# Kernel optimization log

Measured on AMD Instinct MI355X. Metric: run time of the kernel, lower is better.

The kernel has to match this reference:

```python
import jax, jax.numpy as jnp
import numpy as np

TEMPERATURE = 0.5
EPS = 1e-8  # torch CosineSimilarity eps


def setup_inputs() -> dict:
    key = jax.random.key(0)
    # x holds 2*batch_size concatenated embeddings (two augmented views)
    x = jax.random.normal(key, (4096, 512), dtype=jnp.float32)
    return {"x": x}


def reference(x) -> jnp.ndarray:
    n2 = x.shape[0]          # 2N rows
    n = n2 // 2
    # cosine similarity: normalize rows (clamped norm as in torch), then GEMM
    norms = jnp.maximum(jnp.linalg.norm(x, axis=1, keepdims=True), EPS)
    xn = x / norms
    sim = jnp.einsum('id,jd->ij', xn, xn) / TEMPERATURE  # [2N, 2N]
    # positive logit for row i is sim[i, (i+N) mod 2N]
    idx = jnp.arange(n2)
    pos = sim[idx, (idx + n) % n2]
    # CE with label 0 over logits = [pos, negatives]; since the logit set for
    # row i is exactly {sim[i, j] : j != i}, CE_i = logsumexp_{j!=i} sim[i,j] - pos_i
    sim_masked = jnp.where(jnp.eye(n2, dtype=bool), -jnp.inf, sim)
    lse = jax.nn.logsumexp(sim_masked, axis=1)
    # criterion uses reduction='sum' then divides by bsz -> mean
    return jnp.mean(lse - pos)
```

## Files before the change

kernel.cpp:

```cpp
#include <hip/hip_runtime.h>
#include <hip/hip_bf16.h>
#include <math.h>

typedef __bf16 bf16_t;
typedef __bf16 bf16x8 __attribute__((ext_vector_type(8)));
typedef float f32x4 __attribute__((ext_vector_type(4)));

#define N2 4096
#define NHALF 2048
#define DIM 512
#define TEMP_INV 2.0f

__global__ __launch_bounds__(256) void k_prep(const float* __restrict__ x,
                                              bf16_t* __restrict__ xn,
                                              float* __restrict__ pos,
                                              float* __restrict__ diag,
                                              float* __restrict__ rowsum) {
    const int pair = blockIdx.x * 4 + (threadIdx.x >> 6);
    const int lane = threadIdx.x & 63;
    const int rowi = pair;
    const int rowp = pair + NHALF;

    const float4* xi = reinterpret_cast<const float4*>(x + (size_t)rowi * DIM);
    const float4* xp = reinterpret_cast<const float4*>(x + (size_t)rowp * DIM);
    float4 a0 = xi[lane * 2], a1 = xi[lane * 2 + 1];
    float4 b0 = xp[lane * 2], b1 = xp[lane * 2 + 1];

    float ssi = a0.x*a0.x + a0.y*a0.y + a0.z*a0.z + a0.w*a0.w
              + a1.x*a1.x + a1.y*a1.y + a1.z*a1.z + a1.w*a1.w;
    float ssp = b0.x*b0.x + b0.y*b0.y + b0.z*b0.z + b0.w*b0.w
              + b1.x*b1.x + b1.y*b1.y + b1.z*b1.z + b1.w*b1.w;
    float dot = a0.x*b0.x + a0.y*b0.y + a0.z*b0.z + a0.w*b0.w
              + a1.x*b1.x + a1.y*b1.y + a1.z*b1.z + a1.w*b1.w;
#pragma unroll
    for (int off = 32; off; off >>= 1) {
        ssi += __shfl_xor(ssi, off, 64);
        ssp += __shfl_xor(ssp, off, 64);
        dot += __shfl_xor(dot, off, 64);
    }
    const float ni = fmaxf(sqrtf(ssi), 1e-8f);
    const float np = fmaxf(sqrtf(ssp), 1e-8f);
    const float sci = 1.0f / ni, scp = 1.0f / np;

    float va[8] = {a0.x, a0.y, a0.z, a0.w, a1.x, a1.y, a1.z, a1.w};
    float vb[8] = {b0.x, b0.y, b0.z, b0.w, b1.x, b1.y, b1.z, b1.w};
    bf16x8 oi, op;
    float dii = 0.0f, dpp = 0.0f;
#pragma unroll
    for (int t = 0; t < 8; ++t) {
        oi[t] = (bf16_t)(va[t] * sci);
        op[t] = (bf16_t)(vb[t] * scp);
        float fi = (float)oi[t], fp_ = (float)op[t];
        dii += fi * fi;
        dpp += fp_ * fp_;
    }
    *reinterpret_cast<bf16x8*>(xn + (size_t)rowi * DIM + lane * 8) = oi;
    *reinterpret_cast<bf16x8*>(xn + (size_t)rowp * DIM + lane * 8) = op;
#pragma unroll
    for (int off = 32; off; off >>= 1) {
        dii += __shfl_xor(dii, off, 64);
        dpp += __shfl_xor(dpp, off, 64);
    }
    if (lane == 0) {
        const float pv = TEMP_INV * dot * sci * scp;
        pos[rowi] = pv;
        pos[rowp] = pv;
        diag[rowi] = TEMP_INV * dii;
        diag[rowp] = TEMP_INV * dpp;
    }
    if (threadIdx.x < 8) rowsum[blockIdx.x * 8 + threadIdx.x] = 0.0f;
}

__device__ __forceinline__ void load_lds16(const bf16_t* g, bf16_t* l) {
    __builtin_amdgcn_global_load_lds(
        (const __attribute__((address_space(1))) unsigned int*)g,
        (__attribute__((address_space(3))) unsigned int*)l,
        16, 0, 0);
}

__global__ __launch_bounds__(256) void k_simgemm(const bf16_t* __restrict__ xn,
                                                 float* __restrict__ rowsum) {
    __shared__ bf16_t As[128 * 32];
    __shared__ bf16_t Bs[128 * 32];
    __shared__ float  rpA[128];
    __shared__ float  rpB[128];

    const int t = blockIdx.x;
    int bn = (int)((sqrtf(8.0f * (float)t + 1.0f) - 1.0f) * 0.5f);
    while ((bn * (bn + 1)) / 2 > t) --bn;
    while (((bn + 1) * (bn + 2)) / 2 <= t) ++bn;
    const int bm = t - (bn * (bn + 1)) / 2;
    const bool diagb = (bm == bn);

    const int tid  = threadIdx.x;
    const int lane = tid & 63;
    const int wid  = tid >> 6;
    const int wr   = wid >> 1;
    const int wc   = wid & 1;
    const int q    = lane >> 4;
    const int l15  = lane & 15;

    if (tid < 128) { rpA[tid] = 0.0f; rpB[tid] = 0.0f; }

    const int sRow = tid >> 2;
    const int sCol = (tid & 3) * 8;
    const bf16_t* gA0 = xn + (size_t)(bm * 128 + sRow) * DIM + sCol;
    const bf16_t* gB0 = xn + (size_t)(bn * 128 + sRow) * DIM + sCol;
    bf16_t* lA0 = &As[tid * 8];
    bf16_t* lA1 = &As[2048 + tid * 8];
    bf16_t* lB0 = &Bs[tid * 8];
    bf16_t* lB1 = &Bs[2048 + tid * 8];

    f32x4 acc[4][4] = {};

    for (int k0 = 0; k0 < DIM; k0 += 32) {
        __syncthreads();
        load_lds16(gA0 + k0, lA0);
        load_lds16(gA0 + (size_t)64 * DIM + k0, lA1);
        load_lds16(gB0 + k0, lB0);
        load_lds16(gB0 + (size_t)64 * DIM + k0, lB1);
        __syncthreads();

        bf16x8 af[4], bf[4];
#pragma unroll
        for (int mt = 0; mt < 4; ++mt)
            af[mt] = *reinterpret_cast<const bf16x8*>(
                &As[(wr * 64 + mt * 16 + l15) * 32 + q * 8]);
#pragma unroll
        for (int nt = 0; nt < 4; ++nt)
            bf[nt] = *reinterpret_cast<const bf16x8*>(
                &Bs[(wc * 64 + nt * 16 + l15) * 32 + q * 8]);
#pragma unroll
        for (int mt = 0; mt < 4; ++mt)
#pragma unroll
            for (int nt = 0; nt < 4; ++nt)
                acc[mt][nt] = __builtin_amdgcn_mfma_f32_16x16x32_bf16(
                    af[mt], bf[nt], acc[mt][nt], 0, 0, 0);
    }

    float colacc[4] = {0.0f, 0.0f, 0.0f, 0.0f};
#pragma unroll
    for (int mt = 0; mt < 4; ++mt) {
        float rowp[4] = {0.0f, 0.0f, 0.0f, 0.0f};
#pragma unroll
        for (int nt = 0; nt < 4; ++nt)
#pragma unroll
            for (int r = 0; r < 4; ++r) {
                float e = __expf(TEMP_INV * acc[mt][nt][r]);
                rowp[r] += e;
                colacc[nt] += e;
            }
#pragma unroll
        for (int r = 0; r < 4; ++r) {
            float p = rowp[r];
            p += __shfl_xor(p, 1, 64);
            p += __shfl_xor(p, 2, 64);
            p += __shfl_xor(p, 4, 64);
            p += __shfl_xor(p, 8, 64);
            if (l15 == 0) atomicAdd(&rpA[wr * 64 + mt * 16 + q * 4 + r], p);
        }
    }
    if (!diagb) {
#pragma unroll
        for (int nt = 0; nt < 4; ++nt) {
            float c = colacc[nt];
            c += __shfl_xor(c, 16, 64);
            c += __shfl_xor(c, 32, 64);
            if (q == 0) atomicAdd(&rpB[wc * 64 + nt * 16 + l15], c);
        }
    }
    __syncthreads();
    if (tid < 128) {
        atomicAdd(&rowsum[bm * 128 + tid], rpA[tid]);
    } else if (!diagb) {
        atomicAdd(&rowsum[bn * 128 + (tid - 128)], rpB[tid - 128]);
    }
}

__global__ __launch_bounds__(256) void k_finalize(const float* __restrict__ rowsum,
                                                  const float* __restrict__ pos,
                                                  const float* __restrict__ diag,
                                                  float* __restrict__ out) {
    __shared__ float red[256];
    float s = 0.0f;
    for (int i = threadIdx.x; i < N2; i += 256)
        s += __logf(rowsum[i] - __expf(diag[i])) - pos[i];
    red[threadIdx.x] = s;
    __syncthreads();
    for (int st = 128; st; st >>= 1) {
        if (threadIdx.x < st) red[threadIdx.x] += red[threadIdx.x + st];
        __syncthreads();
    }
    if (threadIdx.x == 0) out[0] = red[0] / (float)N2;
}

extern "C" void kernel_launch(void* const* d_in, const int* in_sizes, int n_in,
                              void* d_out, int out_size, void* d_ws, size_t ws_size,
                              hipStream_t stream) {
    (void)in_sizes; (void)n_in; (void)out_size; (void)ws_size;
    const float* x = (const float*)d_in[0];
    float* out = (float*)d_out;

    char* ws = (char*)d_ws;
    bf16_t* xn     = (bf16_t*)ws;
    float*  rowsum = (float*)(ws + (size_t)N2 * DIM * 2);
    float*  pos    = rowsum + N2;
    float*  diag   = pos + N2;

    k_prep<<<512, 256, 0, stream>>>(x, xn, pos, diag, rowsum);
    k_simgemm<<<528, 256, 0, stream>>>(xn, rowsum);
    k_finalize<<<1, 256, 0, stream>>>(rowsum, pos, diag, out);
}
```

Measured before the change: 82.01 us.

## Double-buffer LDS tiles with K=64 in sim GEMM, vectorize finalize loads

The GEMM main loop now loads 64-wide K tiles into two LDS buffers, prefetching the next tile while MFMAs run on the current one. This halves the number of loop iterations and barriers and overlaps global-to-LDS transfers with compute. The cost is four times the LDS footprint (64 KB for the tiles), which may lower occupancy, and the unpadded 64-element row stride may cause LDS bank conflicts. The finalize kernel also reads its inputs as float4 with an unrolled loop.

Result: slower. 87.89 us (+7.2%).

```diff
diff --git a/kernel.cpp b/kernel.cpp
--- a/kernel.cpp
+++ b/kernel.cpp
@@ -80,8 +80,8 @@
 
 __global__ __launch_bounds__(256) void k_simgemm(const bf16_t* __restrict__ xn,
                                                  float* __restrict__ rowsum) {
-    __shared__ bf16_t As[128 * 32];
-    __shared__ bf16_t Bs[128 * 32];
+    __shared__ bf16_t As[2][128 * 64];
+    __shared__ bf16_t Bs[2][128 * 64];
     __shared__ float  rpA[128];
     __shared__ float  rpB[128];
 
@@ -102,40 +102,52 @@
 
     if (tid < 128) { rpA[tid] = 0.0f; rpB[tid] = 0.0f; }
 
-    const int sRow = tid >> 2;
-    const int sCol = (tid & 3) * 8;
-    const bf16_t* gA0 = xn + (size_t)(bm * 128 + sRow) * DIM + sCol;
-    const bf16_t* gB0 = xn + (size_t)(bn * 128 + sRow) * DIM + sCol;
-    bf16_t* lA0 = &As[tid * 8];
-    bf16_t* lA1 = &As[2048 + tid * 8];
-    bf16_t* lB0 = &Bs[tid * 8];
-    bf16_t* lB1 = &Bs[2048 + tid * 8];
+    const int sRow = tid >> 3;
+    const int sCol = (tid & 7) * 8;
+    const bf16_t* gA = xn + (size_t)(bm * 128 + sRow) * DIM + sCol;
+    const bf16_t* gB = xn + (size_t)(bn * 128 + sRow) * DIM + sCol;
 
     f32x4 acc[4][4] = {};
 
-    for (int k0 = 0; k0 < DIM; k0 += 32) {
+#pragma unroll
+    for (int c = 0; c < 4; ++c) {
+        load_lds16(gA + (size_t)(c * 32) * DIM, &As[0][c * 2048 + tid * 8]);
+        load_lds16(gB + (size_t)(c * 32) * DIM, &Bs[0][c * 2048 + tid * 8]);
+    }
+    __syncthreads();
+
+    for (int kt = 0; kt < 8; ++kt) {
+        const int cur = kt & 1;
+        if (kt < 7) {
+            const bf16_t* gA1 = gA + (size_t)(kt + 1) * 64;
+            const bf16_t* gB1 = gB + (size_t)(kt + 1) * 64;
+#pragma unroll
+            for (int c = 0; c < 4; ++c) {
+                load_lds16(gA1 + (size_t)(c * 32) * DIM,
+                           &As[cur ^ 1][c * 2048 + tid * 8]);
+                load_lds16(gB1 + (size_t)(c * 32) * DIM,
+                           &Bs[cur ^ 1][c * 2048 + tid * 8]);
+            }
+        }
+#pragma unroll
+        for (int kk = 0; kk < 2; ++kk) {
+            bf16x8 af[4], bv[4];
+#pragma unroll
+            for (int mt = 0; mt < 4; ++mt)
+                af[mt] = *reinterpret_cast<const bf16x8*>(
+                    &As[cur][(wr * 64 + mt * 16 + l15) * 64 + kk * 32 + q * 8]);
+#pragma unroll
+            for (int nt = 0; nt < 4; ++nt)
+                bv[nt] = *reinterpret_cast<const bf16x8*>(
+                    &Bs[cur][(wc * 64 + nt * 16 + l15) * 64 + kk * 32 + q * 8]);
+#pragma unroll
+            for (int mt = 0; mt < 4; ++mt)
+#pragma unroll
+                for (int nt = 0; nt < 4; ++nt)
+                    acc[mt][nt] = __builtin_amdgcn_mfma_f32_16x16x32_bf16(
+                        af[mt], bv[nt], acc[mt][nt], 0, 0, 0);
+        }
         __syncthreads();
-        load_lds16(gA0 + k0, lA0);
-        load_lds16(gA0 + (size_t)64 * DIM + k0, lA1);
-        load_lds16(gB0 + k0, lB0);
-        load_lds16(gB0 + (size_t)64 * DIM + k0, lB1);
-        __syncthreads();
-
-        bf16x8 af[4], bf[4];
-#pragma unroll
-        for (int mt = 0; mt < 4; ++mt)
-            af[mt] = *reinterpret_cast<const bf16x8*>(
-                &As[(wr * 64 + mt * 16 + l15) * 32 + q * 8]);
-#pragma unroll
-        for (int nt = 0; nt < 4; ++nt)
-            bf[nt] = *reinterpret_cast<const bf16x8*>(
-                &Bs[(wc * 64 + nt * 16 + l15) * 32 + q * 8]);
-#pragma unroll
-        for (int mt = 0; mt < 4; ++mt)
-#pragma unroll
-            for (int nt = 0; nt < 4; ++nt)
-                acc[mt][nt] = __builtin_amdgcn_mfma_f32_16x16x32_bf16(
-                    af[mt], bf[nt], acc[mt][nt], 0, 0, 0);
     }
 
     float colacc[4] = {0.0f, 0.0f, 0.0f, 0.0f};
@@ -182,9 +194,21 @@
                                                   const float* __restrict__ diag,
                                                   float* __restrict__ out) {
     __shared__ float red[256];
+    const float4* rs4 = reinterpret_cast<const float4*>(rowsum);
+    const float4* ps4 = reinterpret_cast<const float4*>(pos);
+    const float4* dg4 = reinterpret_cast<const float4*>(diag);
     float s = 0.0f;
-    for (int i = threadIdx.x; i < N2; i += 256)
-        s += __logf(rowsum[i] - __expf(diag[i])) - pos[i];
+#pragma unroll
+    for (int it = 0; it < 4; ++it) {
+        const int i = it * 256 + threadIdx.x;
+        float4 r = rs4[i];
+        float4 p = ps4[i];
+        float4 d = dg4[i];
+        s += __logf(r.x - __expf(d.x)) - p.x;
+        s += __logf(r.y - __expf(d.y)) - p.y;
+        s += __logf(r.z - __expf(d.z)) - p.z;
+        s += __logf(r.w - __expf(d.w)) - p.w;
+    }
     red[threadIdx.x] = s;
     __syncthreads();
     for (int st = 128; st; st >>= 1) {
```

## Double-buffer GEMM LDS tiles and fuse finalize via last-block counter

Applied to the files above, without the earlier changes.

The sim GEMM now double-buffers its LDS tiles. Each K step issues the next tile's global-to-LDS loads before the MFMAs on the current tile, which leaves one barrier per iteration instead of two. The separate finalize kernel is removed: a global atomic counter picks the last finishing block, and that block does the logsumexp reduction. This drops one kernel launch and aims to hide load latency, at the cost of twice the LDS and some fence and atomic overhead.

Result: slower. 113.1 us (+37.9%).

```diff
diff --git a/kernel.cpp b/kernel.cpp
--- a/kernel.cpp
+++ b/kernel.cpp
@@ -10,12 +10,14 @@
 #define NHALF 2048
 #define DIM 512
 #define TEMP_INV 2.0f
+#define NBLK 528
 
 __global__ __launch_bounds__(256) void k_prep(const float* __restrict__ x,
                                               bf16_t* __restrict__ xn,
                                               float* __restrict__ pos,
                                               float* __restrict__ diag,
-                                              float* __restrict__ rowsum) {
+                                              float* __restrict__ rowsum,
+                                              int* __restrict__ counter) {
     const int pair = blockIdx.x * 4 + (threadIdx.x >> 6);
     const int lane = threadIdx.x & 63;
     const int rowi = pair;
@@ -69,6 +71,7 @@
         diag[rowp] = TEMP_INV * dpp;
     }
     if (threadIdx.x < 8) rowsum[blockIdx.x * 8 + threadIdx.x] = 0.0f;
+    if (blockIdx.x == 0 && threadIdx.x == 8) *counter = 0;
 }
 
 __device__ __forceinline__ void load_lds16(const bf16_t* g, bf16_t* l) {
@@ -79,11 +82,16 @@
 }
 
 __global__ __launch_bounds__(256) void k_simgemm(const bf16_t* __restrict__ xn,
-                                                 float* __restrict__ rowsum) {
-    __shared__ bf16_t As[128 * 32];
-    __shared__ bf16_t Bs[128 * 32];
+                                                 float* __restrict__ rowsum,
+                                                 const float* __restrict__ pos,
+                                                 const float* __restrict__ diag,
+                                                 int* __restrict__ counter,
+                                                 float* __restrict__ out) {
+    __shared__ bf16_t As[2][128 * 32];
+    __shared__ bf16_t Bs[2][128 * 32];
     __shared__ float  rpA[128];
     __shared__ float  rpB[128];
+    __shared__ int    lastBlk;
 
     const int t = blockIdx.x;
     int bn = (int)((sqrtf(8.0f * (float)t + 1.0f) - 1.0f) * 0.5f);
@@ -102,40 +110,43 @@
 
     if (tid < 128) { rpA[tid] = 0.0f; rpB[tid] = 0.0f; }
 
-    const int sRow = tid >> 2;
-    const int sCol = (tid & 3) * 8;
-    const bf16_t* gA0 = xn + (size_t)(bm * 128 + sRow) * DIM + sCol;
-    const bf16_t* gB0 = xn + (size_t)(bn * 128 + sRow) * DIM + sCol;
-    bf16_t* lA0 = &As[tid * 8];
-    bf16_t* lA1 = &As[2048 + tid * 8];
-    bf16_t* lB0 = &Bs[tid * 8];
-    bf16_t* lB1 = &Bs[2048 + tid * 8];
+    const bf16_t* gA = xn + (size_t)(bm * 128 + (tid >> 2)) * DIM + (tid & 3) * 8;
+    const bf16_t* gB = xn + (size_t)(bn * 128 + (tid >> 2)) * DIM + (tid & 3) * 8;
 
     f32x4 acc[4][4] = {};
 
-    for (int k0 = 0; k0 < DIM; k0 += 32) {
-        __syncthreads();
-        load_lds16(gA0 + k0, lA0);
-        load_lds16(gA0 + (size_t)64 * DIM + k0, lA1);
-        load_lds16(gB0 + k0, lB0);
-        load_lds16(gB0 + (size_t)64 * DIM + k0, lB1);
-        __syncthreads();
-
-        bf16x8 af[4], bf[4];
+    load_lds16(gA,                       &As[0][tid * 8]);
+    load_lds16(gA + (size_t)64 * DIM,    &As[0][2048 + tid * 8]);
+    load_lds16(gB,                       &Bs[0][tid * 8]);
+    load_lds16(gB + (size_t)64 * DIM,    &Bs[0][2048 + tid * 8]);
+    __syncthreads();
+
+    for (int kt = 0; kt < 16; ++kt) {
+        const int cur = kt & 1;
+        if (kt < 15) {
+            const bf16_t* gA1 = gA + (size_t)(kt + 1) * 32;
+            const bf16_t* gB1 = gB + (size_t)(kt + 1) * 32;
+            load_lds16(gA1,                    &As[cur ^ 1][tid * 8]);
+            load_lds16(gA1 + (size_t)64 * DIM, &As[cur ^ 1][2048 + tid * 8]);
+            load_lds16(gB1,                    &Bs[cur ^ 1][tid * 8]);
+            load_lds16(gB1 + (size_t)64 * DIM, &Bs[cur ^ 1][2048 + tid * 8]);
+        }
+        bf16x8 af[4], bv[4];
 #pragma unroll
         for (int mt = 0; mt < 4; ++mt)
             af[mt] = *reinterpret_cast<const bf16x8*>(
-                &As[(wr * 64 + mt * 16 + l15) * 32 + q * 8]);
+                &As[cur][(wr * 64 + mt * 16 + l15) * 32 + q * 8]);
 #pragma unroll
         for (int nt = 0; nt < 4; ++nt)
-            bf[nt] = *reinterpret_cast<const bf16x8*>(
-                &Bs[(wc * 64 + nt * 16 + l15) * 32 + q * 8]);
+            bv[nt] = *reinterpret_cast<const bf16x8*>(
+                &Bs[cur][(wc * 64 + nt * 16 + l15) * 32 + q * 8]);
 #pragma unroll
         for (int mt = 0; mt < 4; ++mt)
 #pragma unroll
             for (int nt = 0; nt < 4; ++nt)
                 acc[mt][nt] = __builtin_amdgcn_mfma_f32_16x16x32_bf16(
-                    af[mt], bf[nt], acc[mt][nt], 0, 0, 0);
+                    af[mt], bv[nt], acc[mt][nt], 0, 0, 0);
+        __syncthreads();
     }
 
     float colacc[4] = {0.0f, 0.0f, 0.0f, 0.0f};
@@ -175,23 +186,31 @@
     } else if (!diagb) {
         atomicAdd(&rowsum[bn * 128 + (tid - 128)], rpB[tid - 128]);
     }
-}
-
-__global__ __launch_bounds__(256) void k_finalize(const float* __restrict__ rowsum,
-                                                  const float* __restrict__ pos,
-                                                  const float* __restrict__ diag,
-                                                  float* __restrict__ out) {
-    __shared__ float red[256];
+
+    __threadfence();
+    if (tid == 0) {
+        int prev = atomicAdd(counter, 1);
+        lastBlk = (prev == NBLK - 1);
+    }
+    __syncthreads();
+    if (!lastBlk) return;
+
+    __threadfence();
+    float* red = reinterpret_cast<float*>(As);
     float s = 0.0f;
-    for (int i = threadIdx.x; i < N2; i += 256)
-        s += __logf(rowsum[i] - __expf(diag[i])) - pos[i];
-    red[threadIdx.x] = s;
+#pragma unroll
+    for (int it = 0; it < 16; ++it) {
+        const int i = it * 256 + tid;
+        float r = atomicAdd(&rowsum[i], 0.0f);
+        s += __logf(r - __expf(diag[i])) - pos[i];
+    }
+    red[tid] = s;
     __syncthreads();
     for (int st = 128; st; st >>= 1) {
-        if (threadIdx.x < st) red[threadIdx.x] += red[threadIdx.x + st];
+        if (tid < st) red[tid] += red[tid + st];
         __syncthreads();
     }
-    if (threadIdx.x == 0) out[0] = red[0] / (float)N2;
+    if (tid == 0) out[0] = red[0] / (float)N2;
 }
 
 extern "C" void kernel_launch(void* const* d_in, const int* in_sizes, int n_in,
@@ -206,8 +225,8 @@
     float*  rowsum = (float*)(ws + (size_t)N2 * DIM * 2);
     float*  pos    = rowsum + N2;
     float*  diag   = pos + N2;
-
-    k_prep<<<512, 256, 0, stream>>>(x, xn, pos, diag, rowsum);
-    k_simgemm<<<528, 256, 0, stream>>>(xn, rowsum);
-    k_finalize<<<1, 256, 0, stream>>>(rowsum, pos, diag, out);
-}
+    int*    counter = (int*)(diag + N2);
+
+    k_prep<<<512, 256, 0, stream>>>(x, xn, pos, diag, rowsum, counter);
+    k_simgemm<<<528, 256, 0, stream>>>(xn, rowsum, pos, diag, counter, out);
+}
```
